# Performance work log

Measured on AMD Instinct MI355X. Metric: run time of the kernel, lower is better.

## Reference

```python
import jax, jax.numpy as jnp
import numpy as np
from jax import lax

B, L = 16, 2048
D_TOK, D_TIS = 256, 64
D_MODEL = D_TOK + D_TIS          # 320
EXPAND = 2
D_INNER = EXPAND * D_MODEL       # 640
D_STATE = 16
D_CONV = 4
DT_RANK = (D_MODEL + 15) // 16   # 20 (ceil(d_model/16), Mamba default)
H_OUT = 128
VOCAB = 65                       # len(CODON_MAP_DNA)+1
N_TISSUES = 30
MAX_NORM = 2.0


def _embed_maxnorm(W, idx):
    # torch nn.Embedding(max_norm=2): looked-up rows are renormalized to norm<=2
    e = W[idx]
    n = jnp.linalg.norm(e, axis=-1, keepdims=True)
    return e * jnp.minimum(1.0, MAX_NORM / jnp.maximum(n, 1e-12))


def setup_inputs() -> dict:
    key = jax.random.key(0)
    ks = jax.random.split(key, 18)
    s = 0.02
    seq_W = jax.random.normal(ks[3], (VOCAB, D_TOK), dtype=jnp.float32)
    seq_W = seq_W.at[0].set(0.0)  # padding_idx=0
    A_log = jnp.log(jnp.broadcast_to(jnp.arange(1, D_STATE + 1, dtype=jnp.float32), (D_INNER, D_STATE)))
    return {
        "rna_data_pad": jax.random.randint(ks[0], (B, L), 0, VOCAB).astype(jnp.int32),
        "tissue_id": jax.random.randint(ks[1], (B,), 0, N_TISSUES).astype(jnp.int32),
        "seq_lengths": jax.random.randint(ks[2], (B,), 1, L + 1).astype(jnp.int32),
        "seq_W": seq_W,
        "tissue_W": jax.random.normal(ks[4], (N_TISSUES, D_TIS), dtype=jnp.float32),
        "in_proj_W": jax.random.normal(ks[5], (2 * D_INNER, D_MODEL), dtype=jnp.float32) * s,
        "conv_w": jax.random.normal(ks[6], (D_INNER, 1, D_CONV), dtype=jnp.float32) * s,
        "conv_b": jnp.zeros((D_INNER,), dtype=jnp.float32),
        "x_proj_W": jax.random.normal(ks[7], (DT_RANK + 2 * D_STATE, D_INNER), dtype=jnp.float32) * s,
        "dt_proj_W": jax.random.normal(ks[8], (D_INNER, DT_RANK), dtype=jnp.float32) * s,
        "dt_proj_b": jax.random.uniform(ks[9], (D_INNER,), minval=-4.0, maxval=-2.0),
        "A_log": A_log,
        "D_skip": jnp.ones((D_INNER,), dtype=jnp.float32),
        "out_proj_W": jax.random.normal(ks[10], (D_MODEL, D_INNER), dtype=jnp.float32) * s,
        "p1_W": jax.random.normal(ks[11], (H_OUT, D_MODEL), dtype=jnp.float32) * s,
        "p1_b": jnp.zeros((H_OUT,), dtype=jnp.float32),
        "p2_W": jax.random.normal(ks[12], (1, H_OUT), dtype=jnp.float32) * s,
        "p2_b": jnp.zeros((1,), dtype=jnp.float32),
    }


def reference(rna_data_pad, tissue_id, seq_lengths, seq_W, tissue_W, in_proj_W,
              conv_w, conv_b, x_proj_W, dt_proj_W, dt_proj_b, A_log, D_skip,
              out_proj_W, p1_W, p1_b, p2_W, p2_b):
    b, l = rna_data_pad.shape
    # embeddings + tissue broadcast + mask
    seq_emb = _embed_maxnorm(seq_W, rna_data_pad)            # [B,L,D_TOK]
    tis_emb = _embed_maxnorm(tissue_W, tissue_id)            # [B,D_TIS]
    tis_exp = jnp.broadcast_to(tis_emb[:, None, :], (b, l, tis_emb.shape[-1]))
    x = jnp.concatenate([seq_emb, tis_exp], axis=-1)          # [B,L,D_MODEL]
    x = x * (rna_data_pad != 0)[..., None]
    # Mamba block
    xz = x @ in_proj_W.T                                      # [B,L,2*D_INNER]
    xm, z = jnp.split(xz, 2, axis=-1)
    xt = xm.transpose(0, 2, 1)                                # [B,D_INNER,L]
    conv = lax.conv_general_dilated(
        xt, conv_w, window_strides=(1,), padding=[(D_CONV - 1, 0)],
        feature_group_count=D_INNER,
        dimension_numbers=("NCH", "OIH", "NCH")) + conv_b[None, :, None]
    xm = jax.nn.silu(conv).transpose(0, 2, 1)                 # [B,L,D_INNER]
    x_dbl = xm @ x_proj_W.T                                   # [B,L,DT_RANK+2*D_STATE]
    dt, Bm, Cm = jnp.split(x_dbl, [DT_RANK, DT_RANK + D_STATE], axis=-1)
    delta = jax.nn.softplus(dt @ dt_proj_W.T + dt_proj_b)     # [B,L,D_INNER]
    A = -jnp.exp(A_log)                                       # [D_INNER,D_STATE]
    # selective scan over time
    xs = (delta.transpose(1, 0, 2), Bm.transpose(1, 0, 2),
          Cm.transpose(1, 0, 2), xm.transpose(1, 0, 2))
    h0 = jnp.zeros((b, D_INNER, D_STATE), dtype=xm.dtype)

    def step(h, t):
        dl, bt, ct, ut = t                                    # [B,di],[B,ds],[B,ds],[B,di]
        dA = jnp.exp(dl[:, :, None] * A)                      # [B,di,ds]
        dBu = (dl * ut)[:, :, None] * bt[:, None, :]          # [B,di,ds]
        h = dA * h + dBu
        y = jnp.einsum("bds,bs->bd", h, ct)
        return h, y

    _, ys = lax.scan(step, h0, xs)                            # ys: [L,B,D_INNER]
    y = ys.transpose(1, 0, 2) + xm * D_skip
    y = y * jax.nn.silu(z)
    out = y @ out_proj_W.T                                    # [B,L,D_MODEL]
    # gather last valid timestep
    out_last = out[jnp.arange(b), seq_lengths - 1]            # [B,D_MODEL]
    h1 = jax.nn.relu(out_last @ p1_W.T + p1_b)
    return h1 @ p2_W.T + p2_b                                 # [B,1]
```

## Files before the change

kernel.cpp:

```cpp
#include <hip/hip_runtime.h>
#include <hip/hip_bf16.h>
#include <math.h>

#define B_      16
#define L_      2048
#define D_MODEL 320
#define D_INNER 640
#define D_STATE 16
#define DT_RANK 20
#define H_OUT   128
#define VOCAB   65
#define N_TIS   30
#define TT      8
#define ST      64
#define NCHUNK  16
#define CHLEN   (L_/NCHUNK)
#define NCH2    64
#define CHL2    (L_/NCH2)

static constexpr size_t OFF_MSEQ  = 0;
static constexpr size_t OFF_MTIS  = OFF_MSEQ  + VOCAB*1280;
static constexpr size_t OFF_YSCAN = OFF_MTIS  + N_TIS*1280;
static constexpr size_t OFF_CLAST = OFF_YSCAN + B_*D_INNER;
static constexpr size_t OFF_FLAG  = OFF_CLAST + B_*16;
static constexpr size_t OFF_XDB   = OFF_FLAG  + 16;
static constexpr size_t OFF_PCN   = OFF_XDB  + (size_t)B_*L_*36;
static constexpr size_t OFF_SCN   = OFF_PCN  + (size_t)B_*NCH2*D_INNER;
static constexpr size_t OFF_PC    = OFF_SCN;
static constexpr size_t OFF_SC    = OFF_SCN + (size_t)B_*NCHUNK*40*256;

__device__ __forceinline__ float fast_rcp(float x) { return __builtin_amdgcn_rcpf(x); }
__device__ __forceinline__ float silu_f(float x) { return x * fast_rcp(1.0f + __expf(-x)); }

__global__ __launch_bounds__(256) void k_mbuild(
    const float* __restrict__ seqW, const float* __restrict__ tisW,
    const float* __restrict__ inW, const float* __restrict__ A_log,
    float* __restrict__ ws)
{
    int v = blockIdx.x, tid = threadIdx.x;
    if (v == VOCAB + N_TIS) {
        if (blockIdx.y != 0) return;
        __shared__ int oksh;
        if (tid == 0) oksh = 1;
        __syncthreads();
        int ok = 1;
        for (int i = tid; i < D_INNER*D_STATE; i += 256) {
            int s = i & 15;
            float val = A_log[i];
            if (val != A_log[s]) ok = 0;
            if (i < 16) {
                float a = __expf(val);
                if (fabsf(a - (float)(s+1)) > 1e-3f*(float)(s+1)) ok = 0;
            }
        }
        if (!ok) atomicAnd(&oksh, 0);
        __syncthreads();
        if (tid == 0) ((int*)ws)[OFF_FLAG] = oksh;
        return;
    }

    __shared__ float a_l[256];
    __shared__ float red[4];
    int K, wofs; const float* src; float* dstM;
    if (v < VOCAB) { K = 256; wofs = 0;   src = seqW + (size_t)v*256;        dstM = ws + OFF_MSEQ + (size_t)v*1280; }
    else           { K = 64;  wofs = 256; src = tisW + (size_t)(v-VOCAB)*64; dstM = ws + OFF_MTIS + (size_t)(v-VOCAB)*1280; }
    float x = (tid < K) ? src[tid] : 0.0f;
    float ss = x * x;
    #pragma unroll
    for (int o = 32; o; o >>= 1) ss += __shfl_xor(ss, o);
    if ((tid & 63) == 0) red[tid >> 6] = ss;
    __syncthreads();
    float tot = red[0] + red[1] + red[2] + red[3];
    float scale = fminf(1.0f, 2.0f / fmaxf(sqrtf(tot), 1e-12f));
    a_l[tid] = (tid < K) ? x * scale : 0.0f;
    __syncthreads();

    int wv = tid >> 6, l = tid & 63;
    float4 a4 = ((const float4*)a_l)[l];
    int j0 = blockIdx.y * 256 + wv * 64;
    bool lane_on = (4*l < K);
    for (int jj = 0; jj < 64; jj += 4) {
        float p[4];
        #pragma unroll
        for (int u = 0; u < 4; ++u) {
            float pv = 0.0f;
            if (lane_on) {
                const float4 w4 = *(const float4*)(inW + (size_t)(j0 + jj + u)*320 + wofs + 4*l);
                pv = a4.x*w4.x + a4.y*w4.y + a4.z*w4.z + a4.w*w4.w;
            }
            p[u] = pv;
        }
        float ta, tb;
        ta=__shfl_xor(p[0],1); tb=__shfl_xor(p[1],1); p[0]=(l&1)?(p[1]+tb):(p[0]+ta);
        ta=__shfl_xor(p[2],1); tb=__shfl_xor(p[3],1); p[2]=(l&1)?(p[3]+tb):(p[2]+ta);
        ta=__shfl_xor(p[0],2); tb=__shfl_xor(p[2],2); p[0]=(l&2)?(p[2]+tb):(p[0]+ta);
        p[0]+=__shfl_xor(p[0],4);  p[0]+=__shfl_xor(p[0],8);
        p[0]+=__shfl_xor(p[0],16); p[0]+=__shfl_xor(p[0],32);
        if (l < 4) dstM[j0 + jj + l] = p[0];
    }
}

__global__ __launch_bounds__(256) void k_xdbl(
    const int* __restrict__ idx, const int* __restrict__ tissue_id,
    const int* __restrict__ seq_lengths,
    const float* __restrict__ conv_w, const float* __restrict__ conv_b,
    const float* __restrict__ xW, float* __restrict__ ws)
{
    __shared__ float u_l[TT*641];
    __shared__ float xd_l[TT*36];
    __shared__ int   idx_l[TT+3];
    int b = blockIdx.y;
    int t0 = blockIdx.x * TT;
    int t_last = seq_lengths[b] - 1;
    if (t0 > t_last) return;
    int tid = threadIdx.x;
    const float* Mseq = ws + OFF_MSEQ;
    const float* Mtis = ws + OFF_MTIS;
    int tis = tissue_id[b];
    if (tid < TT+3) {
        int t = t0 - 3 + tid;
        idx_l[tid] = (t >= 0) ? idx[b*L_ + t] : 0;
    }
    __syncthreads();

    for (int d = tid; d < D_INNER; d += 256) {
        float w0 = conv_w[d*4+0], w1 = conv_w[d*4+1], w2 = conv_w[d*4+2], w3 = conv_w[d*4+3];
        float cb = conv_b[d];
        float mt = Mtis[(size_t)tis*1280 + d];
        float xzv[TT+3];
        #pragma unroll
        for (int k = 0; k < TT+3; ++k) {
            unsigned ro = (unsigned)idx_l[k] * 1280u;
            xzv[k] = ro ? (Mseq[ro + (unsigned)d] + mt) : 0.0f;
        }
        #pragma unroll
        for (int t = 0; t < TT; ++t) {
            float c = cb;
            c = fmaf(w0, xzv[t+0], c);
            c = fmaf(w1, xzv[t+1], c);
            c = fmaf(w2, xzv[t+2], c);
            c = fmaf(w3, xzv[t+3], c);
            u_l[t*641 + d] = silu_f(c);
        }
    }
    __syncthreads();

    {
        int w = tid >> 6, l = tid & 63;
        float wreg[9][10];
        #pragma unroll
        for (int kk = 0; kk < 9; ++kk) {
            const float* xr = xW + (size_t)(w + 4*kk)*D_INNER + l;
            #pragma unroll
            for (int i = 0; i < 10; ++i) wreg[kk][i] = xr[64*i];
        }
        for (int t = 0; t < TT; ++t) {
            float p[9];
            #pragma unroll
            for (int kk = 0; kk < 9; ++kk) p[kk] = 0.f;
            #pragma unroll
            for (int i = 0; i < 10; ++i) {
                float ui = u_l[t*641 + l + 64*i];
                #pragma unroll
                for (int kk = 0; kk < 9; ++kk) p[kk] = fmaf(wreg[kk][i], ui, p[kk]);
            }
            {
                float ta, tb;
                ta=__shfl_xor(p[0],1); tb=__shfl_xor(p[1],1); p[0]=(l&1)?(p[1]+tb):(p[0]+ta);
                ta=__shfl_xor(p[2],1); tb=__shfl_xor(p[3],1); p[2]=(l&1)?(p[3]+tb):(p[2]+ta);
                ta=__shfl_xor(p[4],1); tb=__shfl_xor(p[5],1); p[4]=(l&1)?(p[5]+tb):(p[4]+ta);
                ta=__shfl_xor(p[6],1); tb=__shfl_xor(p[7],1); p[6]=(l&1)?(p[7]+tb):(p[6]+ta);
                p[8]+=__shfl_xor(p[8],1);
                ta=__shfl_xor(p[0],2); tb=__shfl_xor(p[2],2); p[0]=(l&2)?(p[2]+tb):(p[0]+ta);
                ta=__shfl_xor(p[4],2); tb=__shfl_xor(p[6],2); p[4]=(l&2)?(p[6]+tb):(p[4]+ta);
                p[8]+=__shfl_xor(p[8],2);
                ta=__shfl_xor(p[0],4); tb=__shfl_xor(p[4],4); p[0]=(l&4)?(p[4]+tb):(p[0]+ta);
                p[8]+=__shfl_xor(p[8],4);
                ta=__shfl_xor(p[0],8); tb=__shfl_xor(p[8],8); p[0]=(l&8)?(p[8]+tb):(p[0]+ta);
                p[0]+=__shfl_xor(p[0],16);
                p[0]+=__shfl_xor(p[0],32);
            }
            if (l < 9) xd_l[t*36 + w + 4*l] = p[0];
        }
        if (t_last < t0 + TT) {
            int tl = t_last - t0;
            float pc[4];
            #pragma unroll
            for (int k = 0; k < 4; ++k) pc[k] = 0.f;
            #pragma unroll
            for (int i = 0; i < 10; ++i) {
                float ui = u_l[tl*641 + l + 64*i];
                #pragma unroll
                for (int k = 0; k < 4; ++k)
                    pc[k] = fmaf(xW[(size_t)(36 + w + 4*k)*D_INNER + l + 64*i], ui, pc[k]);
            }
            #pragma unroll
            for (int o = 32; o; o >>= 1) {
                #pragma unroll
                for (int k = 0; k < 4; ++k) pc[k] += __shfl_xor(pc[k], o);
            }
            if (l == 0) {
                #pragma unroll
                for (int k = 0; k < 4; ++k) ws[OFF_CLAST + b*16 + w + 4*k] = pc[k];
            }
        }
    }
    __syncthreads();

    {
        int nt = min(TT, t_last - t0 + 1);
        int cnt = nt * 36;
        float* dst = ws + OFF_XDB + ((size_t)b*L_ + t0)*36;
        for (int o = tid; o < cnt; o += 256) dst[o] = xd_l[o];
    }
}

__global__ __launch_bounds__(128) void k_scan2(
    const int* __restrict__ idx, const int* __restrict__ tissue_id,
    const int* __restrict__ seq_lengths,
    const float* __restrict__ conv_w, const float* __restrict__ conv_b,
    const float* __restrict__ dtW, const float* __restrict__ dtb,
    float* __restrict__ ws)
{
    if (((const int*)ws)[OFF_FLAG] == 0) return;
    int b = blockIdx.y, c = blockIdx.z;
    int t_last = seq_lengths[b] - 1;
    int t_begin = c * CHL2;
    if (t_begin > t_last) return;
    int t_end = min(t_begin + CHL2 - 1, t_last);
    int d = blockIdx.x * 128 + threadIdx.x;
    unsigned dof = (unsigned)d;
    int tis = tissue_id[b];
    const float* Mseq = ws + OFF_MSEQ;
    const float4* XB  = (const float4*)(ws + OFF_XDB) + (size_t)b*L_*9;
    const int* idxb = idx + b*L_;

    float dtw_r[20];
    #pragma unroll
    for (int i = 0; i < 20; i += 4) {
        float4 w4 = *(const float4*)(dtW + d*20 + i);
        dtw_r[i] = w4.x; dtw_r[i+1] = w4.y; dtw_r[i+2] = w4.z; dtw_r[i+3] = w4.w;
    }
    float4 cw4 = *(const float4*)(conv_w + d*4);
    float  cb  = conv_b[d];
    float  dtb_v = dtb[d];
    float  mt  = ws[OFF_MTIS + (size_t)tis*1280 + d];
    const float L2E = 1.44269504089f;

    auto gath = [&](int t) -> float {
        int row = (t >= 0) ? idxb[t] : 0;
        return row ? (Mseq[(unsigned)row*1280u + dof] + mt) : 0.0f;
    };

    float xw3 = gath(t_end);
    float xw2 = gath(t_end-1);
    float xw1 = gath(t_end-2);
    float xw0 = gath(t_end-3);

    float h[16];
    #pragma unroll
    for (int s = 0; s < 16; ++s) h[s] = 0.f;
    float r = 0.f;

    float4 A0,A1,A2,A3,A4, AB0,AB1,AB2,AB3; float GA;
    float4 E0,E1,E2,E3,E4, EB0,EB1,EB2,EB3; float GE;

#define LOADT(P0,P1,P2,P3,P4,Q0,Q1,Q2,Q3,G,tt) { \
    const float4* _p = XB + (size_t)(tt)*9; \
    P0=_p[0]; P1=_p[1]; P2=_p[2]; P3=_p[3]; P4=_p[4]; \
    Q0=_p[5]; Q1=_p[6]; Q2=_p[7]; Q3=_p[8]; \
    G = gath((tt)-4); }

#define COMPUTE(P0,P1,P2,P3,P4,Q0,Q1,Q2,Q3,G) { \
    float cc = cb; \
    cc = fmaf(cw4.x, xw0, cc); cc = fmaf(cw4.y, xw1, cc); \
    cc = fmaf(cw4.z, xw2, cc); cc = fmaf(cw4.w, xw3, cc); \
    float uu = silu_f(cc); \
    float x = dtb_v; \
    x = fmaf(P0.x, dtw_r[0],  x); x = fmaf(P0.y, dtw_r[1],  x); \
    x = fmaf(P0.z, dtw_r[2],  x); x = fmaf(P0.w, dtw_r[3],  x); \
    x = fmaf(P1.x, dtw_r[4],  x); x = fmaf(P1.y, dtw_r[5],  x); \
    x = fmaf(P1.z, dtw_r[6],  x); x = fmaf(P1.w, dtw_r[7],  x); \
    x = fmaf(P2.x, dtw_r[8],  x); x = fmaf(P2.y, dtw_r[9],  x); \
    x = fmaf(P2.z, dtw_r[10], x); x = fmaf(P2.w, dtw_r[11], x); \
    x = fmaf(P3.x, dtw_r[12], x); x = fmaf(P3.y, dtw_r[13], x); \
    x = fmaf(P3.z, dtw_r[14], x); x = fmaf(P3.w, dtw_r[15], x); \
    x = fmaf(P4.x, dtw_r[16], x); x = fmaf(P4.y, dtw_r[17], x); \
    x = fmaf(P4.z, dtw_r[18], x); x = fmaf(P4.w, dtw_r[19], x); \
    float ee = __expf(-fabsf(x)); \
    float dl = fmaxf(x, 0.0f) + __logf(1.0f + ee); \
    float F  = dl * uu; \
    float p1 = exp2f(-L2E * r); \
    float p2 = p1*p1, p4 = p2*p2, p8 = p4*p4; \
    float q1 = F*p1,  q2 = q1*p1, q3 = q1*p2, q4 = q2*p2; \
    float q5 = q1*p4, q6 = q2*p4, q7 = q3*p4, q8 = q4*p4; \
    float q9 = q1*p8, q10= q2*p8, q11= q3*p8, q12= q4*p8; \
    float q13= q5*p8, q14= q6*p8, q15= q7*p8, q16= q8*p8; \
    h[0]  = fmaf(Q0.x, q1,  h[0]);  h[1]  = fmaf(Q0.y, q2,  h[1]); \
    h[2]  = fmaf(Q0.z, q3,  h[2]);  h[3]  = fmaf(Q0.w, q4,  h[3]); \
    h[4]  = fmaf(Q1.x, q5,  h[4]);  h[5]  = fmaf(Q1.y, q6,  h[5]); \
    h[6]  = fmaf(Q1.z, q7,  h[6]);  h[7]  = fmaf(Q1.w, q8,  h[7]); \
    h[8]  = fmaf(Q2.x, q9,  h[8]);  h[9]  = fmaf(Q2.y, q10, h[9]); \
    h[10] = fmaf(Q2.z, q11, h[10]); h[11] = fmaf(Q2.w, q12, h[11]); \
    h[12] = fmaf(Q3.x, q13, h[12]); h[13] = fmaf(Q3.y, q14, h[13]); \
    h[14] = fmaf(Q3.z, q15, h[14]); h[15] = fmaf(Q3.w, q16, h[15]); \
    r += dl; \
    xw3 = xw2; xw2 = xw1; xw1 = xw0; xw0 = G; }

    int t = t_end;
    LOADT(A0,A1,A2,A3,A4,AB0,AB1,AB2,AB3,GA, t);
    for (;;) {
        int tb = t - 1;
        bool hasB = (tb >= t_begin);
        if (hasB) LOADT(E0,E1,E2,E3,E4,EB0,EB1,EB2,EB3,GE, tb);
        COMPUTE(A0,A1,A2,A3,A4,AB0,AB1,AB2,AB3,GA);
        if (!hasB) break;
        int ta = t - 2;
        bool hasA = (ta >= t_begin);
        if (hasA) LOADT(A0,A1,A2,A3,A4,AB0,AB1,AB2,AB3,GA, ta);
        COMPUTE(E0,E1,E2,E3,E4,EB0,EB1,EB2,EB3,GE);
        if (!hasA) break;
        t = ta;
    }
#undef LOADT
#undef COMPUTE

    ws[OFF_PCN + ((size_t)b*NCH2 + c)*D_INNER + d] = exp2f(-L2E * r);
    float* dst = ws + OFF_SCN + (((size_t)b*NCH2 + c)*D_INNER + d)*16;
    ((float4*)dst)[0] = make_float4(h[0],  h[1],  h[2],  h[3]);
    ((float4*)dst)[1] = make_float4(h[4],  h[5],  h[6],  h[7]);
    ((float4*)dst)[2] = make_float4(h[8],  h[9],  h[10], h[11]);
    ((float4*)dst)[3] = make_float4(h[12], h[13], h[14], h[15]);
}

__global__ __launch_bounds__(256) void k_scanc(
    const int* __restrict__ idx, const int* __restrict__ tissue_id,
    const int* __restrict__ seq_lengths,
    const float* __restrict__ conv_w, const float* __restrict__ conv_b,
    const float* __restrict__ dtW, const float* __restrict__ dtb,
    const float* __restrict__ A_log, float* __restrict__ ws)
{
    if (((const int*)ws)[OFF_FLAG] != 0) return;
    __shared__ float xd_t[ST*20];
    __shared__ float dl_t[16*68];
    __shared__ float du_t[16*68];
    __shared__ float Bb_t[16*68];
    __shared__ float sdred[16*17];
    __shared__ int   idx_t[ST+3];

    int dg = blockIdx.x, b = blockIdx.y, c = blockIdx.z;
    int t_last = seq_lengths[b] - 1;
    int t_begin = c * CHLEN;
    if (t_begin > t_last) return;
    int t_end = min(t_begin + CHLEN - 1, t_last);
    int tid = threadIdx.x;
    int dl = tid >> 4, s = tid & 15;
    int dd = tid & 15, tg = tid >> 4;
    int d_own = dg*16 + dd;
    unsigned dco = (unsigned)d_own;
    int tis = tissue_id[b];
    const float* Mseq = ws + OFF_MSEQ;

    float dtw_r[20];
    #pragma unroll
    for (int i = 0; i < 20; i += 4) {
        float4 w4 = *(const float4*)(dtW + d_own*20 + i);
        dtw_r[i] = w4.x; dtw_r[i+1] = w4.y; dtw_r[i+2] = w4.z; dtw_r[i+3] = w4.w;
    }
    float4 cw4 = *(const float4*)(conv_w + d_own*4);
    float  cb  = conv_b[d_own];
    float  dtb_v = dtb[d_own];
    float  mt  = ws[OFF_MTIS + (size_t)tis*1280 + d_own];
    float As = -__expf(A_log[(dg*16 + dl)*D_STATE + s]) * 1.44269504089f;

    float h = 0.0f;
    float sdp = 0.0f;
    for (int t0 = t_begin; t0 <= t_end; t0 += ST) {
        int nt = min(ST, t_end - t0 + 1);
        if (tid < ST+3) {
            int t = t0 - 3 + tid;
            idx_t[tid] = (t >= 0 && t < L_) ? idx[b*L_ + t] : 0;
        }
        {
            int cnt = nt * 5;
            for (int o = tid; o < cnt; o += 256) {
                int t = o / 5, q = o - t*5;
                ((float4*)xd_t)[o] =
                    *((const float4*)(ws + OFF_XDB) + ((size_t)b*L_ + t0 + t)*9 + q);
            }
        }
        {
            int cnt = nt * 16;
            for (int o = tid; o < cnt; o += 256) {
                int t = o >> 4, sB = o & 15;
                Bb_t[sB*68 + t] = ws[OFF_XDB + ((size_t)b*L_ + t0 + t)*36 + 20 + sB];
            }
        }
        __syncthreads();

        {
            int ttb = tg * 4;
            if (ttb < nt) {
                float xz[7];
                #pragma unroll
                for (int k = 0; k < 7; ++k) {
                    unsigned ro = (unsigned)idx_t[ttb + k] * 1280u;
                    xz[k] = ro ? (Mseq[ro + dco] + mt) : 0.0f;
                }
                float dl4[4], du4[4];
                bool full = (ttb + 3 < nt);
                #pragma unroll
                for (int j = 0; j < 4; ++j) {
                    int tt = ttb + j;
                    if (full || tt < nt) {
                        float cc = cb;
                        cc = fmaf(cw4.x, xz[j+0], cc);
                        cc = fmaf(cw4.y, xz[j+1], cc);
                        cc = fmaf(cw4.z, xz[j+2], cc);
                        cc = fmaf(cw4.w, xz[j+3], cc);
                        float u = silu_f(cc);
                        const float* xr = xd_t + tt*20;
                        float x = dtb_v;
                        #pragma unroll
                        for (int rr = 0; rr < 20; rr += 4) {
                            float4 x4 = *(const float4*)(xr + rr);
                            x = fmaf(x4.x, dtw_r[rr+0], x);
                            x = fmaf(x4.y, dtw_r[rr+1], x);
                            x = fmaf(x4.z, dtw_r[rr+2], x);
                            x = fmaf(x4.w, dtw_r[rr+3], x);
                        }
                        float e = __expf(-fabsf(x));
                        float sp = fmaxf(x, 0.0f) + __logf(1.0f + e);
                        dl4[j] = sp;
                        du4[j] = sp * u;
                        sdp += sp;
                    } else { dl4[j] = 0.f; du4[j] = 0.f; }
                }
                if (full) {
                    *(float4*)(dl_t + dd*68 + ttb) = make_float4(dl4[0], dl4[1], dl4[2], dl4[3]);
                    *(float4*)(du_t + dd*68 + ttb) = make_float4(du4[0], du4[1], du4[2], du4[3]);
                } else {
                    for (int j = 0; j < 4 && ttb + j < nt; ++j) {
                        dl_t[dd*68 + ttb + j] = dl4[j];
                        du_t[dd*68 + ttb + j] = du4[j];
                    }
                }
            }
        }
        __syncthreads();

        {
            int q4 = nt >> 2;
            #pragma unroll 8
            for (int q = 0; q < q4; ++q) {
                float4 d4 = *(const float4*)(dl_t + dl*68 + 4*q);
                float4 u4 = *(const float4*)(du_t + dl*68 + 4*q);
                float4 b4 = *(const float4*)(Bb_t + s*68 + 4*q);
                float e0 = exp2f(d4.x*As), e1 = exp2f(d4.y*As);
                float e2 = exp2f(d4.z*As), e3 = exp2f(d4.w*As);
                float c0 = u4.x*b4.x, c1 = u4.y*b4.y;
                float c2 = u4.z*b4.z, c3 = u4.w*b4.w;
                h = fmaf(e0, h, c0); h = fmaf(e1, h, c1);
                h = fmaf(e2, h, c2); h = fmaf(e3, h, c3);
            }
            for (int tt = q4*4; tt < nt; ++tt) {
                float dlt = dl_t[dl*68 + tt];
                h = fmaf(exp2f(dlt * As), h, du_t[dl*68 + tt] * Bb_t[s*68 + tt]);
            }
        }
        __syncthreads();
    }
    sdred[tg*17 + dd] = sdp;
    __syncthreads();
    float sd = 0.0f;
    #pragma unroll
    for (int g = 0; g < 16; ++g) sd += sdred[g*17 + dl];
    float P = exp2f(As * sd);
    size_t base = (((size_t)b*NCHUNK + c)*40 + dg)*256 + tid;
    ws[OFF_PC + base] = P;
    ws[OFF_SC + base] = h;
}

__global__ __launch_bounds__(256) void k_comb(const int* __restrict__ seq_lengths,
                                              float* __restrict__ ws)
{
    int b = blockIdx.y, dg = blockIdx.x;
    int tid = threadIdx.x;
    int dl = tid >> 4, s = tid & 15;
    int t_last = seq_lengths[b] - 1;
    int flag = ((const int*)ws)[OFF_FLAG];
    float h = 0.0f;
    if (flag) {
        int d = dg*16 + dl;
        int n = s + 1;
        int ncv = t_last / CHL2 + 1;
        const float* Ep = ws + OFF_PCN + (size_t)b*NCH2*D_INNER + d;
        const float* Sp = ws + OFF_SCN + ((size_t)b*NCH2*D_INNER + d)*16 + s;
        for (int c0 = 0; c0 < ncv; c0 += 8) {
            float Ev[8], Sv[8];
            #pragma unroll
            for (int i = 0; i < 8; ++i) {
                bool valid = (c0 + i < ncv);
                Ev[i] = valid ? Ep[(size_t)(c0+i)*D_INNER] : 1.0f;
                Sv[i] = valid ? Sp[(size_t)(c0+i)*D_INNER*16] : 0.0f;
            }
            #pragma unroll
            for (int i = 0; i < 8; ++i) {
                float Es = Ev[i];
                float e2 = Es*Es, e4 = e2*e2, e8 = e4*e4, e16 = e8*e8;
                float W = (n & 1) ? Es : 1.0f;
                W *= (n & 2)  ? e2  : 1.0f;
                W *= (n & 4)  ? e4  : 1.0f;
                W *= (n & 8)  ? e8  : 1.0f;
                W *= (n & 16) ? e16 : 1.0f;
                h = fmaf(W, h, Sv[i]);
            }
        }
    } else {
        int ncv = t_last / CHLEN + 1;
        for (int c = 0; c < ncv; ++c) {
            size_t base = (((size_t)b*NCHUNK + c)*40 + dg)*256 + tid;
            h = fmaf(ws[OFF_PC + base], h, ws[OFF_SC + base]);
        }
    }
    float v = h * ws[OFF_CLAST + b*16 + s];
    v += __shfl_xor(v, 1); v += __shfl_xor(v, 2);
    v += __shfl_xor(v, 4); v += __shfl_xor(v, 8);
    if (s == 0) ws[OFF_YSCAN + (size_t)b*D_INNER + dg*16 + dl] = v;
}

__global__ __launch_bounds__(1024) void k_final(
    const int* __restrict__ idx, const int* __restrict__ tissue_id,
    const int* __restrict__ seq_lengths,
    const float* __restrict__ conv_w, const float* __restrict__ conv_b,
    const float* __restrict__ Dskip, const float* __restrict__ outW,
    const float* __restrict__ p1W, const float* __restrict__ p1b,
    const float* __restrict__ p2W, const float* __restrict__ p2b,
    const float* __restrict__ ws, float* __restrict__ out)
{
    __shared__ float y_l[D_INNER];
    __shared__ float o_l[D_MODEL];
    __shared__ float h1_l[H_OUT];
    int b = blockIdx.x, tid = threadIdx.x;
    int t_last = seq_lengths[b] - 1;
    int tis = tissue_id[b];
    const float* Mseq = ws + OFF_MSEQ;
    const float* Mtis = ws + OFF_MTIS;
    int rows[4];
    #pragma unroll
    for (int k = 0; k < 4; ++k) {
        int t = t_last - 3 + k;
        rows[k] = (t >= 0) ? idx[b*L_ + t] : 0;
    }
    if (tid < D_INNER) {
        int d = tid;
        float conv = conv_b[d];
        const float* cw = conv_w + d*4;
        #pragma unroll
        for (int k = 0; k < 4; ++k) {
            unsigned ro = (unsigned)rows[k] * 1280u;
            float xzv = ro ? (Mseq[ro + (unsigned)d] + Mtis[(size_t)tis*1280 + d]) : 0.0f;
            conv += cw[k] * xzv;
        }
        float u = silu_f(conv);
        unsigned roL = (unsigned)rows[3] * 1280u;
        float z = roL ? (Mseq[roL + 640u + (unsigned)d] + Mtis[(size_t)tis*1280 + 640 + d]) : 0.0f;
        float ys = ws[OFF_YSCAN + (size_t)b*D_INNER + d];
        y_l[d] = (ys + u * Dskip[d]) * silu_f(z);
    }
    __syncthreads();
    {
        int j = tid >> 1, half = tid & 1;
        float acc = 0.f;
        if (j < D_MODEL) {
            const float* w = outW + (size_t)j*D_INNER + half*320;
            const float* y = y_l + half*320;
            #pragma unroll 4
            for (int k = 0; k < 320; k += 4) {
                float4 w4 = *(const float4*)(w + k);
                acc += y[k]*w4.x + y[k+1]*w4.y + y[k+2]*w4.z + y[k+3]*w4.w;
            }
        }
        acc += __shfl_xor(acc, 1);
        if (j < D_MODEL && half == 0) o_l[j] = acc;
    }
    __syncthreads();
    {
        int j = tid >> 3, part = tid & 7;
        float acc = 0.f;
        if (j < H_OUT) {
            const float* w = p1W + (size_t)j*D_MODEL + part*40;
            const float* o = o_l + part*40;
            #pragma unroll
            for (int k = 0; k < 40; k += 4) {
                float4 w4 = *(const float4*)(w + k);
                acc += o[k]*w4.x + o[k+1]*w4.y + o[k+2]*w4.z + o[k+3]*w4.w;
            }
        }
        acc += __shfl_xor(acc, 1); acc += __shfl_xor(acc, 2); acc += __shfl_xor(acc, 4);
        if (j < H_OUT && part == 0) h1_l[j] = fmaxf(acc + p1b[j], 0.0f);
    }
    __syncthreads();
    if (tid < 64) {
        float v = h1_l[tid]*p2W[tid] + h1_l[tid+64]*p2W[tid+64];
        v += __shfl_xor(v, 32); v += __shfl_xor(v, 16); v += __shfl_xor(v, 8);
        v += __shfl_xor(v, 4);  v += __shfl_xor(v, 2);  v += __shfl_xor(v, 1);
        if (tid == 0) out[b] = v + p2b[0];
    }
}

extern "C" void kernel_launch(void* const* d_in, const int* in_sizes, int n_in,
                              void* d_out, int out_size, void* d_ws, size_t ws_size,
                              hipStream_t stream)
{
    const int*   idx   = (const int*)d_in[0];
    const int*   tis   = (const int*)d_in[1];
    const int*   slen  = (const int*)d_in[2];
    const float* seqW  = (const float*)d_in[3];
    const float* tisW  = (const float*)d_in[4];
    const float* inW   = (const float*)d_in[5];
    const float* convw = (const float*)d_in[6];
    const float* convb = (const float*)d_in[7];
    const float* xW    = (const float*)d_in[8];
    const float* dtW   = (const float*)d_in[9];
    const float* dtb   = (const float*)d_in[10];
    const float* Alog  = (const float*)d_in[11];
    const float* Dsk   = (const float*)d_in[12];
    const float* outW  = (const float*)d_in[13];
    const float* p1W   = (const float*)d_in[14];
    const float* p1b   = (const float*)d_in[15];
    const float* p2W   = (const float*)d_in[16];
    const float* p2b   = (const float*)d_in[17];
    float* ws  = (float*)d_ws;
    float* out = (float*)d_out;

    hipLaunchKernelGGL(k_mbuild, dim3(VOCAB + N_TIS + 1, 5), dim3(256), 0, stream,
                       seqW, tisW, inW, Alog, ws);
    hipLaunchKernelGGL(k_xdbl,   dim3(L_/TT, B_),        dim3(256), 0, stream,
                       idx, tis, slen, convw, convb, xW, ws);
    hipLaunchKernelGGL(k_scan2,  dim3(D_INNER/128, B_, NCH2), dim3(128), 0, stream,
                       idx, tis, slen, convw, convb, dtW, dtb, ws);
    hipLaunchKernelGGL(k_scanc,  dim3(D_INNER/16, B_, NCHUNK), dim3(256), 0, stream,
                       idx, tis, slen, convw, convb, dtW, dtb, Alog, ws);
    hipLaunchKernelGGL(k_comb,   dim3(D_INNER/16, B_),   dim3(256), 0, stream, slen, ws);
    hipLaunchKernelGGL(k_final,  dim3(B_),               dim3(1024), 0, stream,
                       idx, tis, slen, convw, convb, Dsk, outW, p1W, p1b, p2W, p2b, ws, out);
}
```

Baseline: 239.8 us.

## Double chunk count, store chunk states in fp16, simplify scan loop

Doubles the number of scan chunks per sequence so each thread handles half as many timesteps, raising the available parallelism in the chunked scan. Chunk-end states are written as half precision, which halves the workspace traffic between the chunk-scan and combine kernels. The manually double-buffered load/compute loop is replaced by a plain loop, leaving scheduling to the compiler. The combine kernel now runs twice as many serial steps, fp16 states lose precision, and the workspace offsets after OFF_SCN were sized for fp32 with the old chunk count, which may overlap.

```diff
diff --git a/kernel.cpp b/kernel.cpp
--- a/kernel.cpp
+++ b/kernel.cpp
@@ -1,5 +1,6 @@
 #include <hip/hip_runtime.h>
 #include <hip/hip_bf16.h>
+#include <hip/hip_fp16.h>
 #include <math.h>
 
 #define B_      16
@@ -15,7 +16,7 @@
 #define ST      64
 #define NCHUNK  16
 #define CHLEN   (L_/NCHUNK)
-#define NCH2    64
+#define NCH2    128
 #define CHL2    (L_/NCH2)
 
 static constexpr size_t OFF_MSEQ  = 0;
@@ -262,75 +263,57 @@
     for (int s = 0; s < 16; ++s) h[s] = 0.f;
     float r = 0.f;
 
-    float4 A0,A1,A2,A3,A4, AB0,AB1,AB2,AB3; float GA;
-    float4 E0,E1,E2,E3,E4, EB0,EB1,EB2,EB3; float GE;
-
-#define LOADT(P0,P1,P2,P3,P4,Q0,Q1,Q2,Q3,G,tt) { \
-    const float4* _p = XB + (size_t)(tt)*9; \
-    P0=_p[0]; P1=_p[1]; P2=_p[2]; P3=_p[3]; P4=_p[4]; \
-    Q0=_p[5]; Q1=_p[6]; Q2=_p[7]; Q3=_p[8]; \
-    G = gath((tt)-4); }
-
-#define COMPUTE(P0,P1,P2,P3,P4,Q0,Q1,Q2,Q3,G) { \
-    float cc = cb; \
-    cc = fmaf(cw4.x, xw0, cc); cc = fmaf(cw4.y, xw1, cc); \
-    cc = fmaf(cw4.z, xw2, cc); cc = fmaf(cw4.w, xw3, cc); \
-    float uu = silu_f(cc); \
-    float x = dtb_v; \
-    x = fmaf(P0.x, dtw_r[0],  x); x = fmaf(P0.y, dtw_r[1],  x); \
-    x = fmaf(P0.z, dtw_r[2],  x); x = fmaf(P0.w, dtw_r[3],  x); \
-    x = fmaf(P1.x, dtw_r[4],  x); x = fmaf(P1.y, dtw_r[5],  x); \
-    x = fmaf(P1.z, dtw_r[6],  x); x = fmaf(P1.w, dtw_r[7],  x); \
-    x = fmaf(P2.x, dtw_r[8],  x); x = fmaf(P2.y, dtw_r[9],  x); \
-    x = fmaf(P2.z, dtw_r[10], x); x = fmaf(P2.w, dtw_r[11], x); \
-    x = fmaf(P3.x, dtw_r[12], x); x = fmaf(P3.y, dtw_r[13], x); \
-    x = fmaf(P3.z, dtw_r[14], x); x = fmaf(P3.w, dtw_r[15], x); \
-    x = fmaf(P4.x, dtw_r[16], x); x = fmaf(P4.y, dtw_r[17], x); \
-    x = fmaf(P4.z, dtw_r[18], x); x = fmaf(P4.w, dtw_r[19], x); \
-    float ee = __expf(-fabsf(x)); \
-    float dl = fmaxf(x, 0.0f) + __logf(1.0f + ee); \
-    float F  = dl * uu; \
-    float p1 = exp2f(-L2E * r); \
-    float p2 = p1*p1, p4 = p2*p2, p8 = p4*p4; \
-    float q1 = F*p1,  q2 = q1*p1, q3 = q1*p2, q4 = q2*p2; \
-    float q5 = q1*p4, q6 = q2*p4, q7 = q3*p4, q8 = q4*p4; \
-    float q9 = q1*p8, q10= q2*p8, q11= q3*p8, q12= q4*p8; \
-    float q13= q5*p8, q14= q6*p8, q15= q7*p8, q16= q8*p8; \
-    h[0]  = fmaf(Q0.x, q1,  h[0]);  h[1]  = fmaf(Q0.y, q2,  h[1]); \
-    h[2]  = fmaf(Q0.z, q3,  h[2]);  h[3]  = fmaf(Q0.w, q4,  h[3]); \
-    h[4]  = fmaf(Q1.x, q5,  h[4]);  h[5]  = fmaf(Q1.y, q6,  h[5]); \
-    h[6]  = fmaf(Q1.z, q7,  h[6]);  h[7]  = fmaf(Q1.w, q8,  h[7]); \
-    h[8]  = fmaf(Q2.x, q9,  h[8]);  h[9]  = fmaf(Q2.y, q10, h[9]); \
-    h[10] = fmaf(Q2.z, q11, h[10]); h[11] = fmaf(Q2.w, q12, h[11]); \
-    h[12] = fmaf(Q3.x, q13, h[12]); h[13] = fmaf(Q3.y, q14, h[13]); \
-    h[14] = fmaf(Q3.z, q15, h[14]); h[15] = fmaf(Q3.w, q16, h[15]); \
-    r += dl; \
-    xw3 = xw2; xw2 = xw1; xw1 = xw0; xw0 = G; }
-
-    int t = t_end;
-    LOADT(A0,A1,A2,A3,A4,AB0,AB1,AB2,AB3,GA, t);
-    for (;;) {
-        int tb = t - 1;
-        bool hasB = (tb >= t_begin);
-        if (hasB) LOADT(E0,E1,E2,E3,E4,EB0,EB1,EB2,EB3,GE, tb);
-        COMPUTE(A0,A1,A2,A3,A4,AB0,AB1,AB2,AB3,GA);
-        if (!hasB) break;
-        int ta = t - 2;
-        bool hasA = (ta >= t_begin);
-        if (hasA) LOADT(A0,A1,A2,A3,A4,AB0,AB1,AB2,AB3,GA, ta);
-        COMPUTE(E0,E1,E2,E3,E4,EB0,EB1,EB2,EB3,GE);
-        if (!hasA) break;
-        t = ta;
-    }
-#undef LOADT
-#undef COMPUTE
+    for (int t = t_end; t >= t_begin; --t) {
+        const float4* _p = XB + (size_t)t*9;
+        float4 P0=_p[0], P1=_p[1], P2=_p[2], P3=_p[3], P4=_p[4];
+        float4 Q0=_p[5], Q1=_p[6], Q2=_p[7], Q3=_p[8];
+        float G = gath(t-4);
+        float cc = cb;
+        cc = fmaf(cw4.x, xw0, cc); cc = fmaf(cw4.y, xw1, cc);
+        cc = fmaf(cw4.z, xw2, cc); cc = fmaf(cw4.w, xw3, cc);
+        float uu = silu_f(cc);
+        float x = dtb_v;
+        x = fmaf(P0.x, dtw_r[0],  x); x = fmaf(P0.y, dtw_r[1],  x);
+        x = fmaf(P0.z, dtw_r[2],  x); x = fmaf(P0.w, dtw_r[3],  x);
+        x = fmaf(P1.x, dtw_r[4],  x); x = fmaf(P1.y, dtw_r[5],  x);
+        x = fmaf(P1.z, dtw_r[6],  x); x = fmaf(P1.w, dtw_r[7],  x);
+        x = fmaf(P2.x, dtw_r[8],  x); x = fmaf(P2.y, dtw_r[9],  x);
+        x = fmaf(P2.z, dtw_r[10], x); x = fmaf(P2.w, dtw_r[11], x);
+        x = fmaf(P3.x, dtw_r[12], x); x = fmaf(P3.y, dtw_r[13], x);
+        x = fmaf(P3.z, dtw_r[14], x); x = fmaf(P3.w, dtw_r[15], x);
+        x = fmaf(P4.x, dtw_r[16], x); x = fmaf(P4.y, dtw_r[17], x);
+        x = fmaf(P4.z, dtw_r[18], x); x = fmaf(P4.w, dtw_r[19], x);
+        float ee = __expf(-fabsf(x));
+        float dl = fmaxf(x, 0.0f) + __logf(1.0f + ee);
+        float F  = dl * uu;
+        float p1 = exp2f(-L2E * r);
+        float p2 = p1*p1, p4 = p2*p2, p8 = p4*p4;
+        float q1 = F*p1,  q2 = q1*p1, q3 = q1*p2, q4 = q2*p2;
+        float q5 = q1*p4, q6 = q2*p4, q7 = q3*p4, q8 = q4*p4;
+        float q9 = q1*p8, q10= q2*p8, q11= q3*p8, q12= q4*p8;
+        float q13= q5*p8, q14= q6*p8, q15= q7*p8, q16= q8*p8;
+        h[0]  = fmaf(Q0.x, q1,  h[0]);  h[1]  = fmaf(Q0.y, q2,  h[1]);
+        h[2]  = fmaf(Q0.z, q3,  h[2]);  h[3]  = fmaf(Q0.w, q4,  h[3]);
+        h[4]  = fmaf(Q1.x, q5,  h[4]);  h[5]  = fmaf(Q1.y, q6,  h[5]);
+        h[6]  = fmaf(Q1.z, q7,  h[6]);  h[7]  = fmaf(Q1.w, q8,  h[7]);
+        h[8]  = fmaf(Q2.x, q9,  h[8]);  h[9]  = fmaf(Q2.y, q10, h[9]);
+        h[10] = fmaf(Q2.z, q11, h[10]); h[11] = fmaf(Q2.w, q12, h[11]);
+        h[12] = fmaf(Q3.x, q13, h[12]); h[13] = fmaf(Q3.y, q14, h[13]);
+        h[14] = fmaf(Q3.z, q15, h[14]); h[15] = fmaf(Q3.w, q16, h[15]);
+        r += dl;
+        xw3 = xw2; xw2 = xw1; xw1 = xw0; xw0 = G;
+    }
 
     ws[OFF_PCN + ((size_t)b*NCH2 + c)*D_INNER + d] = exp2f(-L2E * r);
-    float* dst = ws + OFF_SCN + (((size_t)b*NCH2 + c)*D_INNER + d)*16;
-    ((float4*)dst)[0] = make_float4(h[0],  h[1],  h[2],  h[3]);
-    ((float4*)dst)[1] = make_float4(h[4],  h[5],  h[6],  h[7]);
-    ((float4*)dst)[2] = make_float4(h[8],  h[9],  h[10], h[11]);
-    ((float4*)dst)[3] = make_float4(h[12], h[13], h[14], h[15]);
+    __half2* dst = (__half2*)(ws + OFF_SCN) + (((size_t)b*NCH2 + c)*D_INNER + d)*8;
+    dst[0] = __floats2half2_rn(h[0],  h[1]);
+    dst[1] = __floats2half2_rn(h[2],  h[3]);
+    dst[2] = __floats2half2_rn(h[4],  h[5]);
+    dst[3] = __floats2half2_rn(h[6],  h[7]);
+    dst[4] = __floats2half2_rn(h[8],  h[9]);
+    dst[5] = __floats2half2_rn(h[10], h[11]);
+    dst[6] = __floats2half2_rn(h[12], h[13]);
+    dst[7] = __floats2half2_rn(h[14], h[15]);
 }
 
 __global__ __launch_bounds__(256) void k_scanc(
@@ -495,14 +478,15 @@
         int n = s + 1;
         int ncv = t_last / CHL2 + 1;
         const float* Ep = ws + OFF_PCN + (size_t)b*NCH2*D_INNER + d;
-        const float* Sp = ws + OFF_SCN + ((size_t)b*NCH2*D_INNER + d)*16 + s;
+        const __half* Sp = (const __half*)(ws + OFF_SCN)
+                         + ((size_t)b*NCH2*D_INNER + d)*16 + s;
         for (int c0 = 0; c0 < ncv; c0 += 8) {
             float Ev[8], Sv[8];
             #pragma unroll
             for (int i = 0; i < 8; ++i) {
                 bool valid = (c0 + i < ncv);
                 Ev[i] = valid ? Ep[(size_t)(c0+i)*D_INNER] : 1.0f;
-                Sv[i] = valid ? Sp[(size_t)(c0+i)*D_INNER*16] : 0.0f;
+                Sv[i] = valid ? __half2float(Sp[(size_t)(c0+i)*D_INNER*16]) : 0.0f;
             }
             #pragma unroll
             for (int i = 0; i < 8; ++i) {
```

Measured after the change: 259.0 us. 1.08x slower.
